# Performance work log

Measured on AMD Instinct MI355X. Metric: run time of the kernel, lower is better.

The kernel has to match this reference:

```python
import jax, jax.numpy as jnp
import numpy as np

N_QUBITS = 10
N_QLAYERS = 2
EMBED = 1024
B, S = 16, 1024
DIM = 2 ** N_QUBITS


def _apply_rx(state, theta, w, n):
    # state: [N, 2^n] complex; RX(theta) on wire w (wire 0 = most significant bit)
    nb = state.shape[0]
    left, right = 2 ** w, 2 ** (n - 1 - w)
    psi = state.reshape(nb, left, 2, right)
    t = jnp.asarray(theta, jnp.float32) * 0.5
    c, s = jnp.cos(t), jnp.sin(t)
    if c.ndim == 1:  # per-sample angles
        c, s = c[:, None, None], s[:, None, None]
    a0, a1 = psi[:, :, 0, :], psi[:, :, 1, :]
    n0 = c * a0 - 1j * s * a1
    n1 = -1j * s * a0 + c * a1
    return jnp.stack([n0, n1], axis=2).reshape(nb, -1)


def _apply_cnot(state, c, t, n):
    # CNOT with control wire c, target wire t
    psi = state.reshape((-1,) + (2,) * n)
    ctrl_ax, tgt_ax = c + 1, t + 1
    psi0, psi1 = jnp.split(psi, 2, axis=ctrl_ax)
    psi1 = jnp.flip(psi1, axis=tgt_ax)
    return jnp.concatenate([psi0, psi1], axis=ctrl_ax).reshape(state.shape)


def setup_inputs() -> dict:
    key = jax.random.key(0)
    ks = jax.random.split(key, 6)
    s1 = 1.0 / np.sqrt(EMBED)
    s2 = 1.0 / np.sqrt(N_QUBITS)
    return {
        "x": jax.random.normal(ks[0], (B, S, EMBED), jnp.float32),
        "W1": jax.random.uniform(ks[1], (N_QUBITS, EMBED), jnp.float32, -s1, s1),
        "b1": jax.random.uniform(ks[2], (N_QUBITS,), jnp.float32, -s1, s1),
        "qweights": jax.random.uniform(ks[3], (N_QLAYERS, N_QUBITS), jnp.float32, 0.0, 2.0 * np.pi),
        "W2": jax.random.uniform(ks[4], (EMBED, N_QUBITS), jnp.float32, -s2, s2),
        "b2": jax.random.uniform(ks[5], (EMBED,), jnp.float32, -s2, s2),
    }


def reference(x, W1, b1, qweights, W2, b2):
    n = N_QUBITS
    # linear_1
    ang = (jnp.einsum('bse,qe->bsq', x, W1) + b1).reshape(-1, n)  # [N, n]
    N = ang.shape[0]
    # |0...0> batched state vector
    state = jnp.zeros((N, DIM), jnp.complex64).at[:, 0].set(1.0)
    # AngleEmbedding: RX(ang[:, w]) on each wire
    for w in range(n):
        state = _apply_rx(state, ang[:, w], w, n)
    # BasicEntanglerLayers: RX rotations + CNOT ring per layer
    for l in range(N_QLAYERS):
        for w in range(n):
            state = _apply_rx(state, qweights[l, w], w, n)
        if n == 2:
            state = _apply_cnot(state, 0, 1, n)
        elif n > 2:
            for i in range(n):
                state = _apply_cnot(state, i, (i + 1) % n, n)
    # <Z_w> = sum_idx probs[idx] * (1 - 2*bit_w(idx))
    probs = jnp.real(state * jnp.conj(state))  # [N, 2^n]
    idx = jnp.arange(DIM)
    bits = (idx[:, None] >> (n - 1 - jnp.arange(n))[None, :]) & 1
    signs = (1 - 2 * bits).astype(jnp.float32)  # [2^n, n]
    ev = (probs @ signs).reshape(x.shape[0], x.shape[1], n)  # [B, S, n]
    # linear_2
    return jnp.einsum('bsq,eq->bse', ev, W2) + b2
```

## Files before the change

### kernel.cpp

```cpp
#include <hip/hip_runtime.h>

#define NQ 10
#define EMBED 1024
#define ROWS_PER_BLOCK 32
#define BLOCK 512


constexpr int kPop(int x) { int c = 0; for (int i = 0; i < 10; ++i) c += (x >> i) & 1; return c; }

constexpr int sigma_map(int a) {
    int b = 0;
    for (int i = 0; i < 9; ++i) b |= (((a >> i) & 1) ^ ((a >> (i + 1)) & 1)) << i;
    b |= (((a >> 9) & 1) ^ ((a >> 0) & 1) ^ ((a >> 1) & 1)) << 9;
    return b;
}

#define MAXT 40
struct Terms {
    int nt[NQ];
    int vm[NQ];
    int um[NQ];
    unsigned short tm[NQ][MAXT];
    unsigned short sm[NQ][MAXT];
    float sg[NQ][MAXT];
};

constexpr Terms gen_terms() {
    Terms t{};
    int inv_e[NQ] = {};
    for (int a = 0; a < 1024; ++a) {
        const int s = sigma_map(a);
        for (int q = 0; q < NQ; ++q) if (s == (1 << q)) inv_e[q] = a;
    }
    for (int q = 0; q < NQ; ++q) {
        const int u = inv_e[q];
        int v = 0;
        for (int w = 0; w < NQ; ++w) if ((u >> w) & 1) v ^= inv_e[w];
        t.um[q] = u; t.vm[q] = v;
        int n = 0;
        int S = 0;
        while (true) {
            int T = (((S >> 0) ^ (S >> 9)) & 1)
                  | ((((S >> 0) ^ (S >> 1) ^ (S >> 9)) & 1) << 1);
            for (int j = 2; j < 10; ++j) T |= ((((S >> (j - 1)) ^ (S >> j)) & 1) << j);
            if ((T & ~v) == 0) {
                const int p = kPop(T) + kPop(S);
                if (!(p & 1)) {
                    t.tm[q][n] = (unsigned short)T;
                    t.sm[q][n] = (unsigned short)S;
                    t.sg[q][n] = (p & 2) ? -1.f : 1.f;
                    ++n;
                }
            }
            if (S == u) break;
            S = (S - u) & u;
        }
        t.nt[q] = n;
    }
    return t;
}

constexpr Terms TT = gen_terms();

extern "C" __global__ __launch_bounds__(BLOCK, 4)
void ffq_kernel(const float* __restrict__ x, const float* __restrict__ W1,
                const float* __restrict__ b1, const float* __restrict__ qw,
                const float* __restrict__ W2, const float* __restrict__ b2,
                float* __restrict__ out)
{
    __shared__ float sW1[NQ * EMBED];
    __shared__ float sCA[ROWS_PER_BLOCK][NQ];
    __shared__ float sSA[ROWS_PER_BLOCK][NQ];
    __shared__ float sEV[ROWS_PER_BLOCK][NQ];

    const int tid  = threadIdx.x;
    const int lane = tid & 63;
    const int wv   = tid >> 6;
    const int o    = lane & 15;
    const int g    = lane >> 4;
    const int block0 = blockIdx.x * ROWS_PER_BLOCK;

    {
        const float4* src = (const float4*)W1;
        float4* dst = (float4*)sW1;
        #pragma unroll
        for (int i = 0; i < 5; ++i) dst[tid + BLOCK * i] = src[tid + BLOCK * i];
    }

    float b1r[NQ], qw0[NQ];
    #pragma unroll
    for (int w = 0; w < NQ; ++w) { qw0[w] = qw[w]; b1r[w] = b1[w]; }

    __syncthreads();

    {
        const int rloc = wv * 4 + g;
        const int row  = block0 + rloc;
        float acc[NQ];
        #pragma unroll
        for (int q = 0; q < NQ; ++q) acc[q] = 0.f;

        const float4* xr  = (const float4*)(x + (size_t)row * EMBED);
        const float4* w1v = (const float4*)sW1;
        #pragma unroll 4
        for (int k = 0; k < 16; ++k) {
            const float4 xv = xr[k * 16 + o];
            #pragma unroll
            for (int q = 0; q < NQ; ++q) {
                const float4 wv4 = w1v[q * 256 + k * 16 + o];
                acc[q] = fmaf(xv.x, wv4.x, acc[q]);
                acc[q] = fmaf(xv.y, wv4.y, acc[q]);
                acc[q] = fmaf(xv.z, wv4.z, acc[q]);
                acc[q] = fmaf(xv.w, wv4.w, acc[q]);
            }
        }
        #pragma unroll
        for (int m = 1; m < 16; m <<= 1) {
            #pragma unroll
            for (int q = 0; q < NQ; ++q) acc[q] += __shfl_xor(acc[q], m, 64);
        }
        if (o == 0) {
            #pragma unroll
            for (int w = 0; w < NQ; ++w) {
                const float A = acc[w] + b1r[w] + qw0[w];
                sCA[rloc][w] = __cosf(A);
                sSA[rloc][w] = __sinf(A);
            }
        }
    }

    __syncthreads();

    if (wv < 2 && lane < ROWS_PER_BLOCK) {
        const int row = lane;
        float ca[NQ], sa[NQ], cb[NQ], sb[NQ];
        #pragma unroll
        for (int w = 0; w < NQ; ++w) {
            ca[w] = sCA[row][w];
            sa[w] = sSA[row][w];
            const float B = qw[NQ + w];
            cb[w] = __cosf(B); sb[w] = __sinf(B);
        }
        #define EVQ(QC) do {                                                      \
            float ev = 0.f;                                                       \
            _Pragma("unroll")                                                     \
            for (int k = 0; k < TT.nt[QC]; ++k) {                                 \
                float P = TT.sg[QC][k];                                           \
                _Pragma("unroll")                                                 \
                for (int w = 0; w < NQ; ++w) {                                    \
                    if ((TT.vm[QC] >> w) & 1) P *= ((TT.tm[QC][k] >> w) & 1) ? sa[w] : ca[w]; \
                    if ((TT.um[QC] >> w) & 1) P *= ((TT.sm[QC][k] >> w) & 1) ? sb[w] : cb[w]; \
                }                                                                 \
                ev += P;                                                          \
            }                                                                     \
            sEV[row][QC] = ev;                                                    \
        } while (0)
        if (wv == 0) { EVQ(0); EVQ(9); }
        else         { EVQ(1); EVQ(2); EVQ(3); EVQ(4); EVQ(5); EVQ(6); EVQ(7); EVQ(8); }
        #undef EVQ
    }

    __syncthreads();

    const int e4 = tid & 255;
    const int r0 = (tid >> 8) * 16;

    float w2f[40];
    {
        const float4* w2v = (const float4*)(W2 + e4 * 40);
        #pragma unroll
        for (int i = 0; i < 10; ++i) {
            float4 v = w2v[i];
            w2f[4*i+0] = v.x; w2f[4*i+1] = v.y; w2f[4*i+2] = v.z; w2f[4*i+3] = v.w;
        }
    }
    const float4 b2v = ((const float4*)b2)[e4];

    #pragma unroll
    for (int r = 0; r < 16; ++r) {
        const int rr = r0 + r;
        float evr[NQ];
        #pragma unroll
        for (int q = 0; q < NQ; ++q) evr[q] = sEV[rr][q];
        float o0 = b2v.x, o1 = b2v.y, o2 = b2v.z, o3 = b2v.w;
        #pragma unroll
        for (int q = 0; q < NQ; ++q) {
            o0 = fmaf(evr[q], w2f[ 0 + q], o0);
            o1 = fmaf(evr[q], w2f[10 + q], o1);
            o2 = fmaf(evr[q], w2f[20 + q], o2);
            o3 = fmaf(evr[q], w2f[30 + q], o3);
        }
        float4 ov = {o0, o1, o2, o3};
        ((float4*)(out + (size_t)(block0 + rr) * EMBED))[e4] = ov;
    }
}

extern "C" void kernel_launch(void* const* d_in, const int* in_sizes, int n_in,
                              void* d_out, int out_size, void* d_ws, size_t ws_size,
                              hipStream_t stream) {
    (void)in_sizes; (void)n_in; (void)d_ws; (void)ws_size; (void)out_size;
    const float* x  = (const float*)d_in[0];
    const float* W1 = (const float*)d_in[1];
    const float* b1 = (const float*)d_in[2];
    const float* qw = (const float*)d_in[3];
    const float* W2 = (const float*)d_in[4];
    const float* b2 = (const float*)d_in[5];
    float* out = (float*)d_out;

    const int total_rows = 16 * 1024;
    dim3 grid(total_rows / ROWS_PER_BLOCK);
    ffq_kernel<<<grid, BLOCK, 0, stream>>>(x, W1, b1, qw, W2, b2, out);
}
```

Before: 31.51 us.

## Halve block size, compute two rows per thread group, hoist W2 loads

Measured after the change: 43.29 us. 1.37x slower.

```diff
diff --git a/kernel.cpp b/kernel.cpp
--- a/kernel.cpp
+++ b/kernel.cpp
@@ -3,7 +3,7 @@
 #define NQ 10
 #define EMBED 1024
 #define ROWS_PER_BLOCK 32
-#define BLOCK 512
+#define BLOCK 256
 
 
 constexpr int kPop(int x) { int c = 0; for (int i = 0; i < 10; ++i) c += (x >> i) & 1; return c; }
@@ -62,7 +62,7 @@
 
 constexpr Terms TT = gen_terms();
 
-extern "C" __global__ __launch_bounds__(BLOCK, 4)
+extern "C" __global__ __launch_bounds__(BLOCK, 3)
 void ffq_kernel(const float* __restrict__ x, const float* __restrict__ W1,
                 const float* __restrict__ b1, const float* __restrict__ qw,
                 const float* __restrict__ W2, const float* __restrict__ b2,
@@ -80,58 +80,79 @@
     const int g    = lane >> 4;
     const int block0 = blockIdx.x * ROWS_PER_BLOCK;
 
+    float w2f[40];
+    {
+        const float4* w2v = (const float4*)(W2 + tid * 40);
+        #pragma unroll
+        for (int i = 0; i < 10; ++i) {
+            float4 v = w2v[i];
+            w2f[4*i+0] = v.x; w2f[4*i+1] = v.y; w2f[4*i+2] = v.z; w2f[4*i+3] = v.w;
+        }
+    }
+    const float4 b2v = ((const float4*)b2)[tid];
+
+    float b1r[NQ], qw0[NQ];
+    #pragma unroll
+    for (int w = 0; w < NQ; ++w) { qw0[w] = qw[w]; b1r[w] = b1[w]; }
+
     {
         const float4* src = (const float4*)W1;
         float4* dst = (float4*)sW1;
         #pragma unroll
-        for (int i = 0; i < 5; ++i) dst[tid + BLOCK * i] = src[tid + BLOCK * i];
-    }
-
-    float b1r[NQ], qw0[NQ];
-    #pragma unroll
-    for (int w = 0; w < NQ; ++w) { qw0[w] = qw[w]; b1r[w] = b1[w]; }
-
+        for (int i = 0; i < 10; ++i) dst[tid + BLOCK * i] = src[tid + BLOCK * i];
+    }
     __syncthreads();
 
     {
-        const int rloc = wv * 4 + g;
-        const int row  = block0 + rloc;
-        float acc[NQ];
-        #pragma unroll
-        for (int q = 0; q < NQ; ++q) acc[q] = 0.f;
-
-        const float4* xr  = (const float4*)(x + (size_t)row * EMBED);
+        const int rloc0 = wv * 8 + g * 2;
+        float acc0[NQ], acc1[NQ];
+        #pragma unroll
+        for (int q = 0; q < NQ; ++q) { acc0[q] = 0.f; acc1[q] = 0.f; }
+
+        const float4* xr0 = (const float4*)(x + (size_t)(block0 + rloc0) * EMBED);
+        const float4* xr1 = (const float4*)(x + (size_t)(block0 + rloc0 + 1) * EMBED);
         const float4* w1v = (const float4*)sW1;
         #pragma unroll 4
         for (int k = 0; k < 16; ++k) {
-            const float4 xv = xr[k * 16 + o];
+            const float4 xv0 = xr0[k * 16 + o];
+            const float4 xv1 = xr1[k * 16 + o];
             #pragma unroll
             for (int q = 0; q < NQ; ++q) {
                 const float4 wv4 = w1v[q * 256 + k * 16 + o];
-                acc[q] = fmaf(xv.x, wv4.x, acc[q]);
-                acc[q] = fmaf(xv.y, wv4.y, acc[q]);
-                acc[q] = fmaf(xv.z, wv4.z, acc[q]);
-                acc[q] = fmaf(xv.w, wv4.w, acc[q]);
+                acc0[q] = fmaf(xv0.x, wv4.x, acc0[q]);
+                acc0[q] = fmaf(xv0.y, wv4.y, acc0[q]);
+                acc0[q] = fmaf(xv0.z, wv4.z, acc0[q]);
+                acc0[q] = fmaf(xv0.w, wv4.w, acc0[q]);
+                acc1[q] = fmaf(xv1.x, wv4.x, acc1[q]);
+                acc1[q] = fmaf(xv1.y, wv4.y, acc1[q]);
+                acc1[q] = fmaf(xv1.z, wv4.z, acc1[q]);
+                acc1[q] = fmaf(xv1.w, wv4.w, acc1[q]);
             }
         }
         #pragma unroll
         for (int m = 1; m < 16; m <<= 1) {
             #pragma unroll
-            for (int q = 0; q < NQ; ++q) acc[q] += __shfl_xor(acc[q], m, 64);
+            for (int q = 0; q < NQ; ++q) {
+                acc0[q] += __shfl_xor(acc0[q], m, 64);
+                acc1[q] += __shfl_xor(acc1[q], m, 64);
+            }
         }
         if (o == 0) {
             #pragma unroll
             for (int w = 0; w < NQ; ++w) {
-                const float A = acc[w] + b1r[w] + qw0[w];
-                sCA[rloc][w] = __cosf(A);
-                sSA[rloc][w] = __sinf(A);
+                const float A0 = acc0[w] + b1r[w] + qw0[w];
+                const float A1 = acc1[w] + b1r[w] + qw0[w];
+                sCA[rloc0][w]     = __cosf(A0);
+                sSA[rloc0][w]     = __sinf(A0);
+                sCA[rloc0 + 1][w] = __cosf(A1);
+                sSA[rloc0 + 1][w] = __sinf(A1);
             }
         }
     }
 
     __syncthreads();
 
-    if (wv < 2 && lane < ROWS_PER_BLOCK) {
+    if (lane < ROWS_PER_BLOCK) {
         const int row = lane;
         float ca[NQ], sa[NQ], cb[NQ], sb[NQ];
         #pragma unroll
@@ -155,33 +176,20 @@
             }                                                                     \
             sEV[row][QC] = ev;                                                    \
         } while (0)
-        if (wv == 0) { EVQ(0); EVQ(9); }
-        else         { EVQ(1); EVQ(2); EVQ(3); EVQ(4); EVQ(5); EVQ(6); EVQ(7); EVQ(8); }
+        if      (wv == 0) { EVQ(0); }
+        else if (wv == 1) { EVQ(9); }
+        else if (wv == 2) { EVQ(7); EVQ(8); }
+        else              { EVQ(1); EVQ(2); EVQ(3); EVQ(4); EVQ(5); EVQ(6); }
         #undef EVQ
     }
 
     __syncthreads();
 
-    const int e4 = tid & 255;
-    const int r0 = (tid >> 8) * 16;
-
-    float w2f[40];
-    {
-        const float4* w2v = (const float4*)(W2 + e4 * 40);
-        #pragma unroll
-        for (int i = 0; i < 10; ++i) {
-            float4 v = w2v[i];
-            w2f[4*i+0] = v.x; w2f[4*i+1] = v.y; w2f[4*i+2] = v.z; w2f[4*i+3] = v.w;
-        }
-    }
-    const float4 b2v = ((const float4*)b2)[e4];
-
-    #pragma unroll
-    for (int r = 0; r < 16; ++r) {
-        const int rr = r0 + r;
+    #pragma unroll 4
+    for (int r = 0; r < ROWS_PER_BLOCK; ++r) {
         float evr[NQ];
         #pragma unroll
-        for (int q = 0; q < NQ; ++q) evr[q] = sEV[rr][q];
+        for (int q = 0; q < NQ; ++q) evr[q] = sEV[r][q];
         float o0 = b2v.x, o1 = b2v.y, o2 = b2v.z, o3 = b2v.w;
         #pragma unroll
         for (int q = 0; q < NQ; ++q) {
@@ -191,7 +199,7 @@
             o3 = fmaf(evr[q], w2f[30 + q], o3);
         }
         float4 ov = {o0, o1, o2, o3};
-        ((float4*)(out + (size_t)(block0 + rr) * EMBED))[e4] = ov;
+        ((float4*)(out + (size_t)(block0 + r) * EMBED))[tid] = ov;
     }
 }
 
```
